# Kernel tuning notes

Measured on AMD Instinct MI355X. Metric: run time of the kernel, lower is better.

The kernel has to match this reference:

```python
import jax, jax.numpy as jnp
import numpy as np

N_NODES = 50000
N_EDGES = 400000


def gat(x, src, dst, W, al, ar, b, n):
    # DGL GATConv: fc -> per-head attention logits -> edge softmax over dst -> weighted sum
    heads, dout = al.shape
    z = (x.reshape(-1, x.shape[-1]) @ W.T).reshape(n, heads, dout)   # [N,H,D]
    el = jnp.sum(z * al, axis=-1)                                    # [N,H]
    er = jnp.sum(z * ar, axis=-1)                                    # [N,H]
    e = jax.nn.leaky_relu(el[src] + er[dst], negative_slope=0.2)     # [E,H]
    emax = jax.ops.segment_max(e, dst, num_segments=n)               # [N,H]
    emax = jnp.where(jnp.isfinite(emax), emax, 0.0)                  # zero-in-degree nodes
    ee = jnp.exp(e - emax[dst])
    den = jax.ops.segment_sum(ee, dst, num_segments=n)               # [N,H]
    alpha = ee / den[dst]                                            # edge softmax
    rst = jax.ops.segment_sum(alpha[:, :, None] * z[src], dst, num_segments=n)  # [N,H,D]
    return rst + b.reshape(heads, dout)


def chain_pass(h, src, dst, n):
    # constrainLayer: m_e = z_src - z_dst, sum at dst, then L2-normalize last dim
    m = jax.ops.segment_sum(h[src] - h[dst], dst, num_segments=n)
    l = jnp.sqrt(jnp.sum(m * m, axis=-1, keepdims=True)) + 1e-7
    return m / l


def setup_inputs() -> dict:
    key = jax.random.key(0)
    ks = jax.random.split(key, 32)
    n, e = N_NODES, N_EDGES
    in_dim, hid, out, H = 64, 128, 64, 4

    def nrm(k, shape, s=0.05):
        return jax.random.normal(k, shape, dtype=jnp.float32) * s

    inp = {
        "x": nrm(ks[0], (n, in_dim), 1.0),
        "src0": jax.random.randint(ks[1], (e,), 0, n, dtype=jnp.int32),
        "dst0": jax.random.randint(ks[2], (e,), 0, n, dtype=jnp.int32),
        "src1": jnp.arange(n - 1, dtype=jnp.int32),
        "dst1": jnp.arange(1, n, dtype=jnp.int32),
        # layer1 (in->hid, 1 head) per etype
        "W1a": nrm(ks[3], (hid, in_dim)), "al1a": nrm(ks[4], (1, hid)), "ar1a": nrm(ks[5], (1, hid)), "b1a": nrm(ks[6], (hid,)),
        "W1b": nrm(ks[7], (hid, in_dim)), "al1b": nrm(ks[8], (1, hid)), "ar1b": nrm(ks[9], (1, hid)), "b1b": nrm(ks[10], (hid,)),
        # layer2 (hid->out, 1 head) per etype
        "W2a": nrm(ks[11], (out, hid)), "al2a": nrm(ks[12], (1, out)), "ar2a": nrm(ks[13], (1, out)), "b2a": nrm(ks[14], (out,)),
        "W2b": nrm(ks[15], (out, hid)), "al2b": nrm(ks[16], (1, out)), "ar2b": nrm(ks[17], (1, out)), "b2b": nrm(ks[18], (out,)),
        # layerMH (out->out, H heads) per etype
        "Wma": nrm(ks[19], (H * out, out)), "alma": nrm(ks[20], (H, out)), "arma": nrm(ks[21], (H, out)), "bma": nrm(ks[22], (H * out,)),
        "Wmb": nrm(ks[23], (H * out, out)), "almb": nrm(ks[24], (H, out)), "armb": nrm(ks[25], (H, out)), "bmb": nrm(ks[26], (H * out,)),
        "r": jax.random.uniform(ks[27], (1,), dtype=jnp.float32),
    }
    return inp


def reference(x, src0, dst0, src1, dst1,
              W1a, al1a, ar1a, b1a, W1b, al1b, ar1b, b1b,
              W2a, al2a, ar2a, b2a, W2b, al2b, ar2b, b2b,
              Wma, alma, arma, bma, Wmb, almb, armb, bmb, r):
    n = x.shape[0]
    # HeteroGraphConv(mean) over etypes {interacts, chain}
    h = 0.5 * (gat(x, src0, dst0, W1a, al1a, ar1a, b1a, n)
               + gat(x, src1, dst1, W1b, al1b, ar1b, b1b, n))          # [N,1,hid]
    h = 0.5 * (gat(h, src0, dst0, W2a, al2a, ar2a, b2a, n)
               + gat(h, src1, dst1, W2b, al2b, ar2b, b2b, n))          # [N,1,out]
    radius = jnp.clip(r, 0.01, 3.0)  # computed but unused (dead code in original)
    dh = chain_pass(h, src1, dst1, n)                                   # [N,1,out]
    conh = jnp.cumsum(dh, axis=-2)  # cumsum over singleton head axis (as in original)
    hm = 0.5 * (gat(conh, src0, dst0, Wma, alma, arma, bma, n)
                + gat(conh, src1, dst1, Wmb, almb, armb, bmb, n))       # [N,H,out]
    # per-head chain pass + cumsum over nodes, vectorized across heads
    ds = chain_pass(hm, src1, dst1, n)                                  # [N,H,out]
    res = jnp.cumsum(ds, axis=0)                                        # torch cumsum dim=-2 of [N,out] per head
    return res
```

## Files before the change

kernel.cpp:

```cpp
#include <hip/hip_runtime.h>
#include <math.h>

__device__ __forceinline__ float wred_sum(float v){
  #pragma unroll
  for (int o = 32; o > 0; o >>= 1) v += __shfl_xor(v, o);
  return v;
}
__device__ __forceinline__ float wred_max(float v){
  #pragma unroll
  for (int o = 32; o > 0; o >>= 1) v = fmaxf(v, __shfl_xor(v, o));
  return v;
}
__device__ __forceinline__ float lrelu(float v){ return v > 0.f ? v : 0.2f * v; }

__global__ void k_hist(const int* __restrict__ dst, int* __restrict__ deg, int E){
  int t = blockIdx.x * blockDim.x + threadIdx.x;
  if (t < E) atomicAdd(&deg[dst[t]], 1);
}

__global__ void k_deg_bsum(const int* __restrict__ deg, int* __restrict__ bsum, int n){
  __shared__ int s[256];
  int b = blockIdx.x, t = threadIdx.x;
  int i = b * 256 + t;
  s[t] = (i < n) ? deg[i] : 0;
  __syncthreads();
  for (int o = 128; o > 0; o >>= 1){ if (t < o) s[t] += s[t + o]; __syncthreads(); }
  if (t == 0) bsum[b] = s[0];
}
__global__ void k_bsum_scan(int* __restrict__ bsum, int nblk){
  __shared__ int s[256];
  int t = threadIdx.x;
  s[t] = (t < nblk) ? bsum[t] : 0;
  __syncthreads();
  for (int o = 1; o < 256; o <<= 1){
    int add = (t >= o) ? s[t - o] : 0;
    __syncthreads();
    s[t] += add;
    __syncthreads();
  }
  if (t < nblk) bsum[t] = (t > 0) ? s[t - 1] : 0;
}
__global__ void k_rowptr(const int* __restrict__ deg, const int* __restrict__ bsum,
                         int* __restrict__ rowptr, int* __restrict__ cursor, int n, int E){
  __shared__ int s[256];
  int b = blockIdx.x, t = threadIdx.x;
  int i = b * 256 + t;
  int v = (i < n) ? deg[i] : 0;
  s[t] = v;
  __syncthreads();
  for (int o = 1; o < 256; o <<= 1){
    int add = (t >= o) ? s[t - o] : 0;
    __syncthreads();
    s[t] += add;
    __syncthreads();
  }
  if (i < n){
    int rp = bsum[b] + s[t] - v;
    rowptr[i] = rp;
    cursor[i] = rp;
    if (i == n - 1) rowptr[n] = E;
  }
}

__global__ void k_scatter(const int* __restrict__ src, const int* __restrict__ dst,
                          int* __restrict__ cursor, int* __restrict__ esrc, int E){
  int t = blockIdx.x * blockDim.x + threadIdx.x;
  if (t < E){
    int d = dst[t];
    int p = atomicAdd(&cursor[d], 1);
    esrc[p] = src[t];
  }
}

template<int K, int C, int H>
__global__ void k_gemm(const float* __restrict__ x, const float* __restrict__ W,
                       const float* __restrict__ al, const float* __restrict__ ar,
                       float* __restrict__ z, float* __restrict__ el, float* __restrict__ er,
                       int n){
  constexpr int K4 = K / 4;
  constexpr int CR = C / 64;
  constexpr int CP = C + 1;
  constexpr int R = 8;
  constexpr int ROWS = 4 * R;
  __shared__ float4 WQ[K4 * CP];
  __shared__ float  XS[ROWS][K];

  int t = threadIdx.x;
  int lane = t & 63, wv = t >> 6;
  int rowbase = blockIdx.x * ROWS;

  const float4* W4 = (const float4*)W;
  for (int idx = t; idx < C * K4; idx += 256){
    int c = idx / K4, k4 = idx - c * K4;
    WQ[k4 * CP + c] = W4[idx];
  }
  for (int idx = t; idx < ROWS * K; idx += 256){
    int r = idx / K, k = idx - r * K;
    int row = rowbase + r;
    XS[r][k] = (row < n) ? x[(size_t)row * K + k] : 0.f;
  }
  __syncthreads();

  float acc[R][CR];
  #pragma unroll
  for (int r = 0; r < R; r++)
    #pragma unroll
    for (int j = 0; j < CR; j++) acc[r][j] = 0.f;

  const int r0 = wv * R;
  #pragma unroll 4
  for (int k4 = 0; k4 < K4; k4++){
    float4 wq[CR];
    #pragma unroll
    for (int j = 0; j < CR; j++) wq[j] = WQ[k4 * CP + j * 64 + lane];
    #pragma unroll
    for (int r = 0; r < R; r++){
      float4 xk = *(const float4*)&XS[r0 + r][k4 * 4];
      #pragma unroll
      for (int j = 0; j < CR; j++){
        acc[r][j] += xk.x * wq[j].x;
        acc[r][j] += xk.y * wq[j].y;
        acc[r][j] += xk.z * wq[j].z;
        acc[r][j] += xk.w * wq[j].w;
      }
    }
  }

  float alv[CR], arv[CR];
  if constexpr (H > 0){
    #pragma unroll
    for (int j = 0; j < CR; j++){ alv[j] = al[j * 64 + lane]; arv[j] = ar[j * 64 + lane]; }
  }

  #pragma unroll
  for (int r = 0; r < R; r++){
    int row = rowbase + r0 + r;
    if (row >= n) continue;
    float* zr = z + (size_t)row * C;
    #pragma unroll
    for (int j = 0; j < CR; j++) zr[j * 64 + lane] = acc[r][j];
    if constexpr (H == 1){
      float pl = 0.f, pr = 0.f;
      #pragma unroll
      for (int j = 0; j < CR; j++){ pl += acc[r][j] * alv[j]; pr += acc[r][j] * arv[j]; }
      pl = wred_sum(pl); pr = wred_sum(pr);
      if (lane == 0){ el[row] = pl; er[row] = pr; }
    } else if constexpr (H > 1){
      #pragma unroll
      for (int j = 0; j < CR; j++){
        float pl = wred_sum(acc[r][j] * alv[j]);
        float pr = wred_sum(acc[r][j] * arv[j]);
        if (lane == 0){ el[(size_t)row * H + j] = pl; er[(size_t)row * H + j] = pr; }
      }
    }
  }
}

template<int D>
__global__ void k_gat_h1(const int* __restrict__ rowptr, const int* __restrict__ esrc,
                         const float* __restrict__ z, const float* __restrict__ el,
                         const float* __restrict__ er, const float* __restrict__ b,
                         const float* __restrict__ zb, const float* __restrict__ bb,
                         float* __restrict__ out, int n){
  constexpr int DR = D / 64;
  int lane = threadIdx.x & 63;
  int i = blockIdx.x * (blockDim.x >> 6) + (threadIdx.x >> 6);
  if (i >= n) return;
  int s0 = rowptr[i], s1 = rowptr[i + 1];
  float eri = er[i];
  float m = -INFINITY;
  for (int e = s0 + lane; e < s1; e += 64)
    m = fmaxf(m, lrelu(el[esrc[e]] + eri));
  m = wred_max(m);
  float den = 0.f, den2 = 0.f;
  float acc[DR], acc2[DR];
  #pragma unroll
  for (int j = 0; j < DR; j++){ acc[j] = 0.f; acc2[j] = 0.f; }
  int e = s0;
  for (; e + 1 < s1; e += 2){
    int sA = esrc[e], sB = esrc[e + 1];
    float wA = __expf(lrelu(el[sA] + eri) - m);
    float wB = __expf(lrelu(el[sB] + eri) - m);
    den += wA; den2 += wB;
    const float* zA = z + (size_t)sA * D;
    const float* zB = z + (size_t)sB * D;
    #pragma unroll
    for (int j = 0; j < DR; j++){
      acc[j]  += wA * zA[j * 64 + lane];
      acc2[j] += wB * zB[j * 64 + lane];
    }
  }
  if (e < s1){
    int sA = esrc[e];
    float wA = __expf(lrelu(el[sA] + eri) - m);
    den += wA;
    const float* zA = z + (size_t)sA * D;
    #pragma unroll
    for (int j = 0; j < DR; j++) acc[j] += wA * zA[j * 64 + lane];
  }
  den += den2;
  float inv = (s1 > s0) ? 1.f / den : 0.f;
  float* op = out + (size_t)i * D;
  #pragma unroll
  for (int j = 0; j < DR; j++){
    int c = j * 64 + lane;
    float chain = bb[c];
    if (i > 0) chain += zb[(size_t)(i - 1) * D + c];
    op[c] = 0.5f * (((acc[j] + acc2[j]) * inv + b[c]) + chain);
  }
}

__global__ void k_gat_mh(const int* __restrict__ rowptr, const int* __restrict__ esrc,
                         const float* __restrict__ z, const float* __restrict__ el,
                         const float* __restrict__ er, const float* __restrict__ b,
                         const float* __restrict__ zb, const float* __restrict__ bb,
                         float* __restrict__ out, int n){
  int lane = threadIdx.x & 63;
  int i = blockIdx.x * (blockDim.x >> 6) + (threadIdx.x >> 6);
  if (i >= n) return;
  int s0 = rowptr[i], s1 = rowptr[i + 1];
  const float4 eri = *(const float4*)(er + (size_t)i * 4);
  float m0 = -INFINITY, m1 = -INFINITY, m2 = -INFINITY, m3 = -INFINITY;
  for (int e = s0 + lane; e < s1; e += 64){
    float4 e4 = *(const float4*)(el + (size_t)esrc[e] * 4);
    m0 = fmaxf(m0, lrelu(e4.x + eri.x));
    m1 = fmaxf(m1, lrelu(e4.y + eri.y));
    m2 = fmaxf(m2, lrelu(e4.z + eri.z));
    m3 = fmaxf(m3, lrelu(e4.w + eri.w));
  }
  m0 = wred_max(m0); m1 = wred_max(m1); m2 = wred_max(m2); m3 = wred_max(m3);
  float d0 = 0.f, d1 = 0.f, d2 = 0.f, d3 = 0.f;
  float a0 = 0.f, a1 = 0.f, a2 = 0.f, a3 = 0.f;
  float d0B = 0.f, d1B = 0.f, d2B = 0.f, d3B = 0.f;
  float a0B = 0.f, a1B = 0.f, a2B = 0.f, a3B = 0.f;
  int e = s0;
  for (; e + 1 < s1; e += 2){
    int sA = esrc[e], sB = esrc[e + 1];
    float4 eA = *(const float4*)(el + (size_t)sA * 4);
    float4 eB = *(const float4*)(el + (size_t)sB * 4);
    const float* zA = z + (size_t)sA * 256;
    const float* zB = z + (size_t)sB * 256;
    float w0 = __expf(lrelu(eA.x + eri.x) - m0);
    float w1 = __expf(lrelu(eA.y + eri.y) - m1);
    float w2 = __expf(lrelu(eA.z + eri.z) - m2);
    float w3 = __expf(lrelu(eA.w + eri.w) - m3);
    float v0 = __expf(lrelu(eB.x + eri.x) - m0);
    float v1 = __expf(lrelu(eB.y + eri.y) - m1);
    float v2 = __expf(lrelu(eB.z + eri.z) - m2);
    float v3 = __expf(lrelu(eB.w + eri.w) - m3);
    d0 += w0; d1 += w1; d2 += w2; d3 += w3;
    d0B += v0; d1B += v1; d2B += v2; d3B += v3;
    a0 += w0 * zA[lane];        a0B += v0 * zB[lane];
    a1 += w1 * zA[64 + lane];   a1B += v1 * zB[64 + lane];
    a2 += w2 * zA[128 + lane];  a2B += v2 * zB[128 + lane];
    a3 += w3 * zA[192 + lane];  a3B += v3 * zB[192 + lane];
  }
  if (e < s1){
    int sA = esrc[e];
    float4 eA = *(const float4*)(el + (size_t)sA * 4);
    const float* zA = z + (size_t)sA * 256;
    float w0 = __expf(lrelu(eA.x + eri.x) - m0);
    float w1 = __expf(lrelu(eA.y + eri.y) - m1);
    float w2 = __expf(lrelu(eA.z + eri.z) - m2);
    float w3 = __expf(lrelu(eA.w + eri.w) - m3);
    d0 += w0; d1 += w1; d2 += w2; d3 += w3;
    a0 += w0 * zA[lane];
    a1 += w1 * zA[64 + lane];
    a2 += w2 * zA[128 + lane];
    a3 += w3 * zA[192 + lane];
  }
  d0 += d0B; d1 += d1B; d2 += d2B; d3 += d3B;
  a0 += a0B; a1 += a1B; a2 += a2B; a3 += a3B;
  float has = (s1 > s0) ? 1.f : 0.f;
  a0 = (has != 0.f) ? a0 / d0 : 0.f;
  a1 = (has != 0.f) ? a1 / d1 : 0.f;
  a2 = (has != 0.f) ? a2 / d2 : 0.f;
  a3 = (has != 0.f) ? a3 / d3 : 0.f;
  float* op = out + (size_t)i * 256;
  float av[4] = {a0, a1, a2, a3};
  #pragma unroll
  for (int h = 0; h < 4; h++){
    int c = h * 64 + lane;
    float chain = bb[c];
    if (i > 0) chain += zb[(size_t)(i - 1) * 256 + c];
    op[c] = 0.5f * ((av[h] + b[c]) + chain);
  }
}

__global__ void k_chainpass64(const float* __restrict__ h, float* __restrict__ dh, int n){
  int lane = threadIdx.x & 63;
  int i = blockIdx.x * (blockDim.x >> 6) + (threadIdx.x >> 6);
  if (i >= n) return;
  float d = 0.f;
  if (i > 0) d = h[(size_t)(i - 1) * 64 + lane] - h[(size_t)i * 64 + lane];
  float ss = wred_sum(d * d);
  dh[(size_t)i * 64 + lane] = d / (sqrtf(ss) + 1e-7f);
}

__global__ void k_chainpass_mh(const float* __restrict__ hm, float* __restrict__ ds, int n){
  int lane = threadIdx.x & 63;
  int i = blockIdx.x * (blockDim.x >> 6) + (threadIdx.x >> 6);
  if (i >= n) return;
  const float* cur = hm + (size_t)i * 256;
  const float* prv = hm + (size_t)(i - 1) * 256;
  #pragma unroll
  for (int h = 0; h < 4; h++){
    int c = h * 64 + lane;
    float d = (i > 0) ? (prv[c] - cur[c]) : 0.f;
    float ss = wred_sum(d * d);
    ds[(size_t)i * 256 + c] = d / (sqrtf(ss) + 1e-7f);
  }
}

__global__ void k_chunk_sum(const float* __restrict__ ds, float* __restrict__ csum, int n, int ch){
  int b = blockIdx.x, t = threadIdx.x;
  int r0 = b * ch, r1 = r0 + ch; if (r1 > n) r1 = n;
  float s = 0.f;
  for (int r = r0; r < r1; r++) s += ds[(size_t)r * 256 + t];
  csum[(size_t)b * 256 + t] = s;
}
__global__ void k_scan_chunks_par(float* __restrict__ csum, int nb){
  __shared__ float s[512];
  int col = blockIdx.x;
  int t = threadIdx.x;
  s[t] = (t < nb) ? csum[(size_t)t * 256 + col] : 0.f;
  __syncthreads();
  #pragma unroll
  for (int o = 1; o < 512; o <<= 1){
    float add = (t >= o) ? s[t - o] : 0.f;
    __syncthreads();
    s[t] += add;
    __syncthreads();
  }
  if (t < nb) csum[(size_t)t * 256 + col] = (t > 0) ? s[t - 1] : 0.f;
}
__global__ void k_apply_scan(float* __restrict__ ds, const float* __restrict__ csum, int n, int ch){
  int b = blockIdx.x, t = threadIdx.x;
  int r0 = b * ch, r1 = r0 + ch; if (r1 > n) r1 = n;
  float run = csum[(size_t)b * 256 + t];
  for (int r = r0; r < r1; r++){
    run += ds[(size_t)r * 256 + t];
    ds[(size_t)r * 256 + t] = run;
  }
}

extern "C" void kernel_launch(void* const* d_in, const int* in_sizes, int n_in,
                              void* d_out, int out_size, void* d_ws, size_t ws_size,
                              hipStream_t stream){
  const float* x    = (const float*)d_in[0];
  const int*   src0 = (const int*)d_in[1];
  const int*   dst0 = (const int*)d_in[2];
  const float* W1a  = (const float*)d_in[5];
  const float* al1a = (const float*)d_in[6];
  const float* ar1a = (const float*)d_in[7];
  const float* b1a  = (const float*)d_in[8];
  const float* W1b  = (const float*)d_in[9];
  const float* b1b  = (const float*)d_in[12];
  const float* W2a  = (const float*)d_in[13];
  const float* al2a = (const float*)d_in[14];
  const float* ar2a = (const float*)d_in[15];
  const float* b2a  = (const float*)d_in[16];
  const float* W2b  = (const float*)d_in[17];
  const float* b2b  = (const float*)d_in[20];
  const float* Wma  = (const float*)d_in[21];
  const float* alma = (const float*)d_in[22];
  const float* arma = (const float*)d_in[23];
  const float* bma  = (const float*)d_in[24];
  const float* Wmb  = (const float*)d_in[25];
  const float* bmb  = (const float*)d_in[28];

  const int n = in_sizes[0] / 64;
  const int E = in_sizes[1];
  const size_t nf = (size_t)n;

  float* ws  = (float*)d_ws;
  float* A   = ws;
  float* B   = A + nf * 256;
  float* C   = B + nf * 256;
  float* D2  = C + nf * 256;
  float* E2  = D2 + nf * 64;
  float* ela = E2 + nf * 64;
  float* era = ela + nf * 4;
  const int ch = 100;
  const int nb = (n + ch - 1) / ch;
  float* csum = era + nf * 4;
  int* deg    = (int*)(csum + (size_t)nb * 256);
  int* rowptr = deg + n;
  int* cursor = rowptr + (n + 1);
  int* esrc   = cursor + n;
  int* bsum   = esrc + E;

  float* dsout = (float*)d_out;

  const int nwb  = (n + 3) / 4;
  const int ngb  = (n + 31) / 32;
  const int eb   = (E + 255) / 256;
  const int nblk = (n + 255) / 256;

  hipMemsetAsync(deg, 0, (size_t)n * sizeof(int), stream);
  k_hist<<<eb, 256, 0, stream>>>(dst0, deg, E);
  k_deg_bsum<<<nblk, 256, 0, stream>>>(deg, bsum, n);
  k_bsum_scan<<<1, 256, 0, stream>>>(bsum, nblk);
  k_rowptr<<<nblk, 256, 0, stream>>>(deg, bsum, rowptr, cursor, n, E);
  k_scatter<<<eb, 256, 0, stream>>>(src0, dst0, cursor, esrc, E);

  k_gemm<64, 128, 1><<<ngb, 256, 0, stream>>>(x, W1a, al1a, ar1a, A, ela, era, n);
  k_gemm<64, 128, 0><<<ngb, 256, 0, stream>>>(x, W1b, nullptr, nullptr, B, nullptr, nullptr, n);
  k_gat_h1<128><<<nwb, 256, 0, stream>>>(rowptr, esrc, A, ela, era, b1a, B, b1b, C, n);

  k_gemm<128, 64, 1><<<ngb, 256, 0, stream>>>(C, W2a, al2a, ar2a, A, ela, era, n);
  k_gemm<128, 64, 0><<<ngb, 256, 0, stream>>>(C, W2b, nullptr, nullptr, B, nullptr, nullptr, n);
  k_gat_h1<64><<<nwb, 256, 0, stream>>>(rowptr, esrc, A, ela, era, b2a, B, b2b, D2, n);

  k_chainpass64<<<nwb, 256, 0, stream>>>(D2, E2, n);

  k_gemm<64, 256, 4><<<ngb, 256, 0, stream>>>(E2, Wma, alma, arma, A, ela, era, n);
  k_gemm<64, 256, 0><<<ngb, 256, 0, stream>>>(E2, Wmb, nullptr, nullptr, B, nullptr, nullptr, n);
  k_gat_mh<<<nwb, 256, 0, stream>>>(rowptr, esrc, A, ela, era, bma, B, bmb, C, n);

  k_chainpass_mh<<<nwb, 256, 0, stream>>>(C, dsout, n);

  k_chunk_sum<<<nb, 256, 0, stream>>>(dsout, csum, n, ch);
  k_scan_chunks_par<<<256, 512, 0, stream>>>(csum, nb);
  k_apply_scan<<<nb, 256, 0, stream>>>(dsout, csum, n, ch);
}
```

Baseline: 762.9 us.

## Fuse paired etype GEMMs into one kernel and fold attention vectors into weights

Replaces the two separate GEMM launches per layer (etype a and b) with a single kernel that loads each input tile once into shared memory and computes both projections. The attention logits el/er are no longer reduced from z with wavefront shuffles. They are computed as a third small GEMM against precomputed vectors W^T·al and W^T·ar, produced by a tiny setup kernel. The aim is to halve the reads of the input activations and cut launches. The cost is smaller per-chunk weight tiles with more __syncthreads, fewer accumulators per thread, and a wasted 64-column pass for only 2H useful columns.

Result: faster. 718.2 us (-5.9%).

```diff
diff --git a/kernel.cpp b/kernel.cpp
--- a/kernel.cpp
+++ b/kernel.cpp
@@ -72,85 +72,123 @@
   }
 }
 
+__global__ void k_valvar_all(const float* __restrict__ W1, const float* __restrict__ al1, const float* __restrict__ ar1,
+                             const float* __restrict__ W2, const float* __restrict__ al2, const float* __restrict__ ar2,
+                             const float* __restrict__ Wm, const float* __restrict__ alm, const float* __restrict__ arm,
+                             float* __restrict__ vv1, float* __restrict__ vv2, float* __restrict__ vvm){
+  int b = blockIdx.x, k = threadIdx.x;
+  if (b == 0){
+    if (k < 64){
+      float v = 0.f, w = 0.f;
+      for (int c = 0; c < 128; c++){ float ww = W1[c * 64 + k]; v += al1[c] * ww; w += ar1[c] * ww; }
+      vv1[k] = v; vv1[64 + k] = w;
+    }
+  } else if (b == 1){
+    float v = 0.f, w = 0.f;
+    for (int c = 0; c < 64; c++){ float ww = W2[c * 128 + k]; v += al2[c] * ww; w += ar2[c] * ww; }
+    vv2[k] = v; vv2[128 + k] = w;
+  } else {
+    if (k < 64){
+      for (int h = 0; h < 4; h++){
+        float v = 0.f, w = 0.f;
+        for (int c = 0; c < 64; c++){
+          float ww = Wm[(size_t)(h * 64 + c) * 64 + k];
+          v += alm[h * 64 + c] * ww; w += arm[h * 64 + c] * ww;
+        }
+        vvm[(2 * h) * 64 + k] = v; vvm[(2 * h + 1) * 64 + k] = w;
+      }
+    }
+  }
+}
+
 template<int K, int C, int H>
-__global__ void k_gemm(const float* __restrict__ x, const float* __restrict__ W,
-                       const float* __restrict__ al, const float* __restrict__ ar,
-                       float* __restrict__ z, float* __restrict__ el, float* __restrict__ er,
-                       int n){
-  constexpr int K4 = K / 4;
-  constexpr int CR = C / 64;
-  constexpr int CP = C + 1;
-  constexpr int R = 8;
-  constexpr int ROWS = 4 * R;
-  __shared__ float4 WQ[K4 * CP];
+__global__ void k_gemm2(const float* __restrict__ x,
+                        const float* __restrict__ Wa, const float* __restrict__ Wb,
+                        const float* __restrict__ vv,
+                        float* __restrict__ za, float* __restrict__ zb,
+                        float* __restrict__ el, float* __restrict__ er, int n){
+  constexpr int K4 = K / 4, NKC = K / 64, NCC = C / 64;
+  constexpr int ROWS = 16384 / (K * 4);
+  constexpr int RPW = ROWS / 4;
   __shared__ float  XS[ROWS][K];
-
-  int t = threadIdx.x;
-  int lane = t & 63, wv = t >> 6;
+  __shared__ float4 WQ[16 * 65];
+
+  int t = threadIdx.x, lane = t & 63, wv = t >> 6;
   int rowbase = blockIdx.x * ROWS;
 
-  const float4* W4 = (const float4*)W;
-  for (int idx = t; idx < C * K4; idx += 256){
-    int c = idx / K4, k4 = idx - c * K4;
-    WQ[k4 * CP + c] = W4[idx];
-  }
-  for (int idx = t; idx < ROWS * K; idx += 256){
-    int r = idx / K, k = idx - r * K;
+  for (int idx = t; idx < 1024; idx += 256){
+    int r = idx / K4, k4 = idx - r * K4;
     int row = rowbase + r;
-    XS[r][k] = (row < n) ? x[(size_t)row * K + k] : 0.f;
-  }
-  __syncthreads();
-
-  float acc[R][CR];
-  #pragma unroll
-  for (int r = 0; r < R; r++)
+    float4 v = make_float4(0.f, 0.f, 0.f, 0.f);
+    if (row < n) v = *(const float4*)&x[(size_t)row * K + k4 * 4];
+    *(float4*)&XS[r][k4 * 4] = v;
+  }
+
+  const int r0 = wv * RPW;
+  float acc[RPW];
+
+  for (int m = 0; m < 2; m++){
+    const float* W = m ? Wb : Wa;
+    float* z = m ? zb : za;
+    for (int cc = 0; cc < NCC; cc++){
+      #pragma unroll
+      for (int r = 0; r < RPW; r++) acc[r] = 0.f;
+      for (int kc = 0; kc < NKC; kc++){
+        __syncthreads();
+        const float4* W4 = (const float4*)W;
+        for (int idx = t; idx < 1024; idx += 256){
+          int c = idx >> 4, k4 = idx & 15;
+          WQ[k4 * 65 + c] = W4[(size_t)(cc * 64 + c) * K4 + kc * 16 + k4];
+        }
+        __syncthreads();
+        #pragma unroll 4
+        for (int k4 = 0; k4 < 16; k4++){
+          float4 wq = WQ[k4 * 65 + lane];
+          #pragma unroll
+          for (int r = 0; r < RPW; r++){
+            float4 xk = *(const float4*)&XS[r0 + r][kc * 64 + k4 * 4];
+            acc[r] += xk.x * wq.x + xk.y * wq.y + xk.z * wq.z + xk.w * wq.w;
+          }
+        }
+      }
+      #pragma unroll
+      for (int r = 0; r < RPW; r++){
+        int row = rowbase + r0 + r;
+        if (row < n) z[(size_t)row * C + cc * 64 + lane] = acc[r];
+      }
+    }
+  }
+
+  {
     #pragma unroll
-    for (int j = 0; j < CR; j++) acc[r][j] = 0.f;
-
-  const int r0 = wv * R;
-  #pragma unroll 4
-  for (int k4 = 0; k4 < K4; k4++){
-    float4 wq[CR];
-    #pragma unroll
-    for (int j = 0; j < CR; j++) wq[j] = WQ[k4 * CP + j * 64 + lane];
-    #pragma unroll
-    for (int r = 0; r < R; r++){
-      float4 xk = *(const float4*)&XS[r0 + r][k4 * 4];
+    for (int r = 0; r < RPW; r++) acc[r] = 0.f;
+    for (int kc = 0; kc < NKC; kc++){
+      __syncthreads();
+      const float4* V4 = (const float4*)vv;
+      for (int idx = t; idx < 1024; idx += 256){
+        int c = idx >> 4, k4 = idx & 15;
+        float4 v = make_float4(0.f, 0.f, 0.f, 0.f);
+        if (c < 2 * H) v = V4[(size_t)c * K4 + kc * 16 + k4];
+        WQ[k4 * 65 + c] = v;
+      }
+      __syncthreads();
+      #pragma unroll 4
+      for (int k4 = 0; k4 < 16; k4++){
+        float4 wq = WQ[k4 * 65 + lane];
+        #pragma unroll
+        for (int r = 0; r < RPW; r++){
+          float4 xk = *(const float4*)&XS[r0 + r][kc * 64 + k4 * 4];
+          acc[r] += xk.x * wq.x + xk.y * wq.y + xk.z * wq.z + xk.w * wq.w;
+        }
+      }
+    }
+    if (lane < 2 * H){
+      int h = lane >> 1;
+      float* dst = (lane & 1) ? er : el;
       #pragma unroll
-      for (int j = 0; j < CR; j++){
-        acc[r][j] += xk.x * wq[j].x;
-        acc[r][j] += xk.y * wq[j].y;
-        acc[r][j] += xk.z * wq[j].z;
-        acc[r][j] += xk.w * wq[j].w;
-      }
-    }
-  }
-
-  float alv[CR], arv[CR];
-  if constexpr (H > 0){
-    #pragma unroll
-    for (int j = 0; j < CR; j++){ alv[j] = al[j * 64 + lane]; arv[j] = ar[j * 64 + lane]; }
-  }
-
-  #pragma unroll
-  for (int r = 0; r < R; r++){
-    int row = rowbase + r0 + r;
-    if (row >= n) continue;
-    float* zr = z + (size_t)row * C;
-    #pragma unroll
-    for (int j = 0; j < CR; j++) zr[j * 64 + lane] = acc[r][j];
-    if constexpr (H == 1){
-      float pl = 0.f, pr = 0.f;
-      #pragma unroll
-      for (int j = 0; j < CR; j++){ pl += acc[r][j] * alv[j]; pr += acc[r][j] * arv[j]; }
-      pl = wred_sum(pl); pr = wred_sum(pr);
-      if (lane == 0){ el[row] = pl; er[row] = pr; }
-    } else if constexpr (H > 1){
-      #pragma unroll
-      for (int j = 0; j < CR; j++){
-        float pl = wred_sum(acc[r][j] * alv[j]);
-        float pr = wred_sum(acc[r][j] * arv[j]);
-        if (lane == 0){ el[(size_t)row * H + j] = pl; er[(size_t)row * H + j] = pr; }
+      for (int r = 0; r < RPW; r++){
+        int row = rowbase + r0 + r;
+        if (row < n) dst[(size_t)row * H + h] = acc[r];
       }
     }
   }
@@ -389,11 +427,13 @@
   int* cursor = rowptr + (n + 1);
   int* esrc   = cursor + n;
   int* bsum   = esrc + E;
+  float* vv1  = (float*)(bsum + 256);
+  float* vv2  = vv1 + 128;
+  float* vvm  = vv2 + 256;
 
   float* dsout = (float*)d_out;
 
   const int nwb  = (n + 3) / 4;
-  const int ngb  = (n + 31) / 32;
   const int eb   = (E + 255) / 256;
   const int nblk = (n + 255) / 256;
 
@@ -404,18 +444,18 @@
   k_rowptr<<<nblk, 256, 0, stream>>>(deg, bsum, rowptr, cursor, n, E);
   k_scatter<<<eb, 256, 0, stream>>>(src0, dst0, cursor, esrc, E);
 
-  k_gemm<64, 128, 1><<<ngb, 256, 0, stream>>>(x, W1a, al1a, ar1a, A, ela, era, n);
-  k_gemm<64, 128, 0><<<ngb, 256, 0, stream>>>(x, W1b, nullptr, nullptr, B, nullptr, nullptr, n);
+  k_valvar_all<<<3, 128, 0, stream>>>(W1a, al1a, ar1a, W2a, al2a, ar2a, Wma, alma, arma,
+                                      vv1, vv2, vvm);
+
+  k_gemm2<64, 128, 1><<<(n + 63) / 64, 256, 0, stream>>>(x, W1a, W1b, vv1, A, B, ela, era, n);
   k_gat_h1<128><<<nwb, 256, 0, stream>>>(rowptr, esrc, A, ela, era, b1a, B, b1b, C, n);
 
-  k_gemm<128, 64, 1><<<ngb, 256, 0, stream>>>(C, W2a, al2a, ar2a, A, ela, era, n);
-  k_gemm<128, 64, 0><<<ngb, 256, 0, stream>>>(C, W2b, nullptr, nullptr, B, nullptr, nullptr, n);
+  k_gemm2<128, 64, 1><<<(n + 31) / 32, 256, 0, stream>>>(C, W2a, W2b, vv2, A, B, ela, era, n);
   k_gat_h1<64><<<nwb, 256, 0, stream>>>(rowptr, esrc, A, ela, era, b2a, B, b2b, D2, n);
 
   k_chainpass64<<<nwb, 256, 0, stream>>>(D2, E2, n);
 
-  k_gemm<64, 256, 4><<<ngb, 256, 0, stream>>>(E2, Wma, alma, arma, A, ela, era, n);
-  k_gemm<64, 256, 0><<<ngb, 256, 0, stream>>>(E2, Wmb, nullptr, nullptr, B, nullptr, nullptr, n);
+  k_gemm2<64, 256, 4><<<(n + 63) / 64, 256, 0, stream>>>(E2, Wma, Wmb, vvm, A, B, ela, era, n);
   k_gat_mh<<<nwb, 256, 0, stream>>>(rowptr, esrc, A, ela, era, bma, B, bmb, C, n);
 
   k_chainpass_mh<<<nwb, 256, 0, stream>>>(C, dsout, n);
```
